# Optimization experiments

Hardware: AMD Instinct MI355X
Metric: run time of the kernel (lower is better)

Reference implementation:

```python
import jax, jax.numpy as jnp
import numpy as np

N_NODES = 50000
N_EDGES = 1600000
F_NODE = 128
F_EDGE = 64
L = 128
EPS = 1e-5


def _bn(h, gamma, beta):
    # BatchNorm1d in training mode: biased batch stats over dim 0
    mu = jnp.mean(h, axis=0, keepdims=True)
    var = jnp.mean((h - mu) ** 2, axis=0, keepdims=True)
    return (h - mu) * jax.lax.rsqrt(var + EPS) * gamma + beta


def setup_inputs() -> dict:
    key = jax.random.key(0)
    ks = jax.random.split(key, 12)
    e1 = F_NODE + F_EDGE          # 192
    e2 = F_NODE + L               # 256
    inp = {
        "x": jax.random.normal(ks[0], (N_NODES, F_NODE), jnp.float32),
        "edge_index": jax.random.randint(ks[1], (2, N_EDGES), 0, N_NODES, jnp.int32),
        "edge_attr": jax.random.normal(ks[2], (N_EDGES, F_EDGE), jnp.float32),
        "u": jax.random.normal(ks[3], (1, 4), jnp.float32),
        "batch": jnp.zeros((N_NODES,), jnp.int32),
        # node_mlp_1: Linear(192 -> 128) + BN + ReLU
        "W1": jax.random.normal(ks[4], (e1, L), jnp.float32) / np.sqrt(e1),
        "b1": jnp.zeros((L,), jnp.float32),
        "g1": jnp.ones((L,), jnp.float32),
        "be1": jnp.zeros((L,), jnp.float32),
        # node_mlp_2: Linear(256 -> 256) + BN + ReLU
        "W2": jax.random.normal(ks[5], (e2, e2), jnp.float32) / np.sqrt(e2),
        "b2": jnp.zeros((e2,), jnp.float32),
        "g2": jnp.ones((e2,), jnp.float32),
        "be2": jnp.zeros((e2,), jnp.float32),
        # linear: 256 -> 128
        "Wl": jax.random.normal(ks[6], (e2, F_NODE), jnp.float32) / np.sqrt(e2),
        "bl": jnp.zeros((F_NODE,), jnp.float32),
    }
    return inp


def reference(x, edge_index, edge_attr, u, batch, W1, b1, g1, be1, W2, b2, g2, be2, Wl, bl):
    n = x.shape[0]
    row, col = edge_index[0], edge_index[1]
    # gather source node feats, concat with edge feats -> [E, F_NODE+F_EDGE]
    h = jnp.concatenate([x[row], edge_attr], axis=1)
    h = jax.nn.relu(_bn(h @ W1 + b1, g1, be1))        # [E, L]
    # scatter-mean over destination nodes
    s = jax.ops.segment_sum(h, col, num_segments=n)   # [N, L]
    cnt = jax.ops.segment_sum(jnp.ones((h.shape[0], 1), h.dtype), col, num_segments=n)
    agg = jnp.where(cnt > 0, s / jnp.maximum(cnt, 1.0), 0.0)
    h2 = jnp.concatenate([x, agg], axis=1)            # [N, F_NODE+L]
    h2 = jax.nn.relu(_bn(h2 @ W2 + b2, g2, be2))
    return jax.nn.relu(h2 @ Wl + bl)                  # [N, F_NODE]
```

## Files before the change

kernel.cpp:

```cpp
#include <hip/hip_runtime.h>
#include <stdint.h>

#define EPSV 1e-5f

typedef short short8 __attribute__((ext_vector_type(8)));
typedef float floatx4 __attribute__((ext_vector_type(4)));

static __device__ __forceinline__ ushort f2b(float f) {
    union { float f; uint32_t u; } v; v.f = f;
    return (ushort)((v.u + 0x7FFFu + ((v.u >> 16) & 1u)) >> 16);
}
static __device__ __forceinline__ uint pack2(float a, float b) {
    return (uint)f2b(a) | ((uint)f2b(b) << 16);
}
static __device__ __forceinline__ float b2f(ushort b) {
    union { uint32_t u; float f; } v; v.u = ((uint32_t)b) << 16;
    return v.f;
}

__global__ void k_prep_w(const float* __restrict__ W, ushort* __restrict__ Wt,
                         int K, int Nc) {
    int i = blockIdx.x * blockDim.x + threadIdx.x;
    if (i >= K * Nc) return;
    int n = i % Nc, k = i / Nc;
    Wt[(size_t)n * K + k] = f2b(W[i]);
}

__global__ void k_prep_x(const float* __restrict__ x, ushort* __restrict__ xb, int n4) {
    int stride = gridDim.x * blockDim.x;
    for (int i = blockIdx.x * blockDim.x + threadIdx.x; i < n4; i += stride) {
        float4 v = ((const float4*)x)[i];
        uint2 o; o.x = pack2(v.x, v.y); o.y = pack2(v.z, v.w);
        ((uint2*)xb)[i] = o;
    }
}

__global__ void k_hist(const int* __restrict__ col, int* __restrict__ deg, int E) {
    int stride = gridDim.x * blockDim.x;
    for (int i = blockIdx.x * blockDim.x + threadIdx.x; i < E; i += stride)
        atomicAdd(&deg[col[i]], 1);
}

__global__ void k_bsum(const int* __restrict__ deg, int* __restrict__ bsum, int Nn) {
    __shared__ int red[256];
    int t = threadIdx.x;
    int i = blockIdx.x * 256 + t;
    red[t] = (i < Nn) ? deg[i] : 0;
    __syncthreads();
    for (int s = 128; s > 0; s >>= 1) {
        if (t < s) red[t] += red[t + s];
        __syncthreads();
    }
    if (t == 0) bsum[blockIdx.x] = red[0];
}

__global__ void k_bscan(const int* __restrict__ bsum, int* __restrict__ bbase, int NB) {
    __shared__ int s[256];
    int t = threadIdx.x;
    int v = (t < NB) ? bsum[t] : 0;
    s[t] = v;
    __syncthreads();
    for (int off = 1; off < 256; off <<= 1) {
        int u = (t >= off) ? s[t - off] : 0;
        __syncthreads();
        s[t] += u;
        __syncthreads();
    }
    if (t < NB) bbase[t] = s[t] - v;
}

__global__ void k_base(const int* __restrict__ deg, const int* __restrict__ bbase,
                       int* __restrict__ base, int Nn) {
    __shared__ int s[256];
    int t = threadIdx.x;
    int i = blockIdx.x * 256 + t;
    int v = (i < Nn) ? deg[i] : 0;
    s[t] = v;
    __syncthreads();
    for (int off = 1; off < 256; off <<= 1) {
        int u = (t >= off) ? s[t - off] : 0;
        __syncthreads();
        s[t] += u;
        __syncthreads();
    }
    if (i < Nn) base[i] = bbase[blockIdx.x] + s[t] - v;
}

__global__ void k_scatter(const int* __restrict__ eidx, const int* __restrict__ base,
                          int* __restrict__ fill, int* __restrict__ perm,
                          int* __restrict__ srcs, int* __restrict__ dsts, int E) {
    int stride = gridDim.x * blockDim.x;
    for (int e = blockIdx.x * blockDim.x + threadIdx.x; e < E; e += stride) {
        int d = eidx[E + e];
        int pos = base[d] + atomicAdd(&fill[d], 1);
        perm[pos] = e;
        if (srcs) { srcs[pos] = eidx[e]; dsts[pos] = d; }
    }
}

__global__ void k_fin(const float* __restrict__ stats, const float* __restrict__ g,
                      const float* __restrict__ be, float* __restrict__ ss,
                      int C, float invM) {
    int c = blockIdx.x * blockDim.x + threadIdx.x;
    if (c >= C) return;
    float mean = stats[c] * invM;
    float var  = stats[C + c] * invM - mean * mean;
    float scale = g[c] * rsqrtf(var + EPSV);
    ss[c] = scale;
    ss[C + c] = be[c] - mean * scale;
}

__global__ void k_fin1(const float* __restrict__ statsB, const float* __restrict__ g,
                       const float* __restrict__ be, float* __restrict__ ss, float invM) {
    int c = threadIdx.x;
    float sm = 0.f, sq = 0.f;
    for (int b = 0; b < 128; ++b) {
        sm += statsB[b * 256 + c];
        sq += statsB[b * 256 + 128 + c];
    }
    float mean = sm * invM;
    float var  = sq * invM - mean * mean;
    float scale = g[c] * rsqrtf(var + EPSV);
    ss[c] = scale;
    ss[128 + c] = be[c] - mean * scale;
}

template <bool BF>
__global__ __launch_bounds__(256) void k_xa(
    const ushort* __restrict__ xb, const ushort* __restrict__ W1t,
    void* __restrict__ out, int Nn)
{
    __shared__ ushort sA[128][72];
    __shared__ ushort sB[128][72];
    const int tid = threadIdx.x;
    const int lane = tid & 63, wave = tid >> 6;
    const int q = lane >> 4, lm = lane & 15;
    const int wr = wave * 32;
    const int rs = tid >> 1;
    const int kh = (tid & 1) * 32;
    const int m0 = blockIdx.x * 128;
    const int row = m0 + rs;
    const bool valid = row < Nn;

    floatx4 acc[2][8];
#pragma unroll
    for (int a = 0; a < 2; ++a)
#pragma unroll
        for (int b = 0; b < 8; ++b) acc[a][b] = (floatx4){0.f, 0.f, 0.f, 0.f};

#pragma unroll
    for (int kc = 0; kc < 2; ++kc) {
        uint4* dstA = (uint4*)&sA[rs][kh];
        const uint4* srcA = (const uint4*)(xb + (size_t)row * 128 + kc * 64 + kh);
#pragma unroll
        for (int j = 0; j < 4; ++j) {
            uint4 o = {0u, 0u, 0u, 0u};
            if (valid) o = srcA[j];
            dstA[j] = o;
        }
        const uint4* srcB = (const uint4*)(W1t + (size_t)rs * 192 + kc * 64 + kh);
        uint4* dstB = (uint4*)&sB[rs][kh];
#pragma unroll
        for (int j = 0; j < 4; ++j) dstB[j] = srcB[j];
        __syncthreads();
#pragma unroll
        for (int ks = 0; ks < 2; ++ks) {
            short8 a0 = *(const short8*)&sA[wr + lm][ks * 32 + q * 8];
            short8 a1 = *(const short8*)&sA[wr + 16 + lm][ks * 32 + q * 8];
#pragma unroll
            for (int ct = 0; ct < 8; ++ct) {
                short8 b = *(const short8*)&sB[ct * 16 + lm][ks * 32 + q * 8];
                acc[0][ct] = __builtin_amdgcn_mfma_f32_16x16x32_bf16(a0, b, acc[0][ct], 0, 0, 0);
                acc[1][ct] = __builtin_amdgcn_mfma_f32_16x16x32_bf16(a1, b, acc[1][ct], 0, 0, 0);
            }
        }
        __syncthreads();
    }
#pragma unroll
    for (int rt = 0; rt < 2; ++rt)
#pragma unroll
        for (int r = 0; r < 4; ++r) {
            int grow = m0 + wr + rt * 16 + q * 4 + r;
            if (grow < Nn) {
                if (BF) {
                    ushort* drow = (ushort*)out + (size_t)grow * 128;
#pragma unroll
                    for (int ct = 0; ct < 8; ++ct)
                        drow[ct * 16 + lm] = f2b(acc[rt][ct][r]);
                } else {
                    float* drow = (float*)out + (size_t)grow * 128;
#pragma unroll
                    for (int ct = 0; ct < 8; ++ct)
                        drow[ct * 16 + lm] = acc[rt][ct][r];
                }
            }
        }
}

__global__ __launch_bounds__(256) void k_edgeA(
    const float* __restrict__ ea, const int* __restrict__ perm,
    const int* __restrict__ srcs, const ushort* __restrict__ W1t,
    const ushort* __restrict__ xab, float* __restrict__ statsB,
    ushort* __restrict__ hs, int E, int NT)
{
    __shared__ union SM {
        struct { ushort A[128][72]; ushort B[128][72]; } t;
        ushort X[128][132];
    } sm;
    __shared__ int sPE[128];
    __shared__ int sSrc[128];
    __shared__ float sRed[256];

    const int tid = threadIdx.x;
    const int lane = tid & 63, wave = tid >> 6;
    const int q = lane >> 4, lm = lane & 15;
    const int wr = wave * 32;
    const int rs = tid >> 1;
    const int half = tid & 1;
    const int kh = half * 32;

    float s1[8], s2[8];
#pragma unroll
    for (int ct = 0; ct < 8; ++ct) { s1[ct] = 0.f; s2[ct] = 0.f; }

    for (int tile = blockIdx.x; tile < NT; tile += gridDim.x) {
        const int e0 = tile * 128;
        __syncthreads();
        if (tid < 128) {
            int e = e0 + tid;
            sPE[tid]  = (e < E) ? perm[e] : -1;
            sSrc[tid] = (e < E) ? srcs[e] : -1;
        }
        __syncthreads();
        {
            int pe = sPE[rs];
            const float4* srcA = (const float4*)(ea + (size_t)pe * 64 + kh);
            uint4* dstA = (uint4*)&sm.t.A[rs][kh];
#pragma unroll
            for (int j = 0; j < 4; ++j) {
                uint4 o = {0u, 0u, 0u, 0u};
                if (pe >= 0) {
                    float4 v0 = srcA[2 * j], v1 = srcA[2 * j + 1];
                    o.x = pack2(v0.x, v0.y); o.y = pack2(v0.z, v0.w);
                    o.z = pack2(v1.x, v1.y); o.w = pack2(v1.z, v1.w);
                }
                dstA[j] = o;
            }
            const uint4* srcB = (const uint4*)(W1t + (size_t)rs * 192 + 128 + kh);
            uint4* dstB = (uint4*)&sm.t.B[rs][kh];
#pragma unroll
            for (int j = 0; j < 4; ++j) dstB[j] = srcB[j];
        }
        __syncthreads();

        floatx4 acc[2][8];
#pragma unroll
        for (int a = 0; a < 2; ++a)
#pragma unroll
            for (int b = 0; b < 8; ++b) acc[a][b] = (floatx4){0.f, 0.f, 0.f, 0.f};
#pragma unroll
        for (int ks = 0; ks < 2; ++ks) {
            short8 a0 = *(const short8*)&sm.t.A[wr + lm][ks * 32 + q * 8];
            short8 a1 = *(const short8*)&sm.t.A[wr + 16 + lm][ks * 32 + q * 8];
#pragma unroll
            for (int ct = 0; ct < 8; ++ct) {
                short8 b = *(const short8*)&sm.t.B[ct * 16 + lm][ks * 32 + q * 8];
                acc[0][ct] = __builtin_amdgcn_mfma_f32_16x16x32_bf16(a0, b, acc[0][ct], 0, 0, 0);
                acc[1][ct] = __builtin_amdgcn_mfma_f32_16x16x32_bf16(a1, b, acc[1][ct], 0, 0, 0);
            }
        }
        __syncthreads();
        {
            int s = sSrc[rs];
            const uint4* gsrc = (const uint4*)(xab + (size_t)(s < 0 ? 0 : s) * 128 + half * 64);
            uint2* ldst = (uint2*)((char*)&sm.X[rs][0] + half * 128);
#pragma unroll
            for (int j = 0; j < 8; ++j) {
                uint4 v = {0u, 0u, 0u, 0u};
                if (s >= 0) v = gsrc[j];
                ldst[2 * j]     = (uint2){v.x, v.y};
                ldst[2 * j + 1] = (uint2){v.z, v.w};
            }
        }
        __syncthreads();
#pragma unroll
        for (int rt = 0; rt < 2; ++rt)
#pragma unroll
            for (int r = 0; r < 4; ++r) {
                int trow = wr + rt * 16 + q * 4 + r;
                if (sPE[trow] >= 0) {
                    ushort* drow = hs + (size_t)(e0 + trow) * 128;
#pragma unroll
                    for (int ct = 0; ct < 8; ++ct) {
                        float v = acc[rt][ct][r] + b2f(sm.X[trow][ct * 16 + lm]);
                        s1[ct] += v; s2[ct] += v * v;
                        drow[ct * 16 + lm] = f2b(v);
                    }
                }
            }
    }

    __syncthreads();
    sRed[tid] = 0.f;
    __syncthreads();
#pragma unroll
    for (int ct = 0; ct < 8; ++ct) {
        float sm2 = s1[ct], sq2 = s2[ct];
        sm2 += __shfl_xor(sm2, 16, 64); sm2 += __shfl_xor(sm2, 32, 64);
        sq2 += __shfl_xor(sq2, 16, 64); sq2 += __shfl_xor(sq2, 32, 64);
        if (q == 0) {
            atomicAdd(&sRed[ct * 16 + lm], sm2);
            atomicAdd(&sRed[128 + ct * 16 + lm], sq2);
        }
    }
    __syncthreads();
    atomicAdd(&statsB[(size_t)(blockIdx.x & 127) * 256 + tid], sRed[tid]);
}

__global__ __launch_bounds__(256) void k_edgeB(
    const ushort* __restrict__ hs, const int* __restrict__ dsts,
    const float* __restrict__ ss, float* __restrict__ sacc, int E, int NT)
{
    __shared__ int sDst[128];
    const int tid = threadIdx.x;
    const int c = tid & 127;
    const int chunk = tid >> 7;
    const float sc = ss[c], sh = ss[128 + c];

    for (int tile = blockIdx.x; tile < NT; tile += gridDim.x) {
        const int e0 = tile * 128;
        __syncthreads();
        if (tid < 128) {
            int e = e0 + tid;
            sDst[tid] = (e < E) ? dsts[e] : -1;
        }
        __syncthreads();
        const int rbeg = chunk * 64;
        int cur = sDst[rbeg];
        float run = 0.f;
#pragma unroll 4
        for (int i = 0; i < 64; ++i) {
            int d = sDst[rbeg + i];
            float v = 0.f;
            if (d >= 0) {
                float hv = b2f(hs[(size_t)(e0 + rbeg + i) * 128 + c]);
                v = fmaxf(fmaf(hv, sc, sh), 0.f);
            }
            if (d != cur) {
                if (cur >= 0) atomicAdd(&sacc[(size_t)cur * 128 + c], run);
                run = 0.f; cur = d;
            }
            run += v;
        }
        if (cur >= 0) atomicAdd(&sacc[(size_t)cur * 128 + c], run);
    }
}

__global__ __launch_bounds__(256) void k_edge1(
    const float* __restrict__ ea, const int* __restrict__ eidx,
    const ushort* __restrict__ W1t, const float* __restrict__ xa,
    float* __restrict__ statsB, int E, int NT)
{
    __shared__ ushort sA[128][72];
    __shared__ ushort sB[128][72];
    __shared__ int sSrc[128];
    __shared__ float sRed[256];

    const int tid = threadIdx.x;
    const int lane = tid & 63, wave = tid >> 6;
    const int q = lane >> 4, lm = lane & 15;
    const int wr = wave * 32;
    const int rs = tid >> 1;
    const int kh = (tid & 1) * 32;

    {
        const uint4* srcB = (const uint4*)(W1t + (size_t)rs * 192 + 128 + kh);
        uint4* dstB = (uint4*)&sB[rs][kh];
#pragma unroll
        for (int j = 0; j < 4; ++j) dstB[j] = srcB[j];
    }

    float s1[8], s2[8];
#pragma unroll
    for (int ct = 0; ct < 8; ++ct) { s1[ct] = 0.f; s2[ct] = 0.f; }

    for (int tile = blockIdx.x; tile < NT; tile += gridDim.x) {
        const int e0 = tile * 128;
        __syncthreads();
        if (tid < 128) {
            int e = e0 + tid;
            sSrc[tid] = (e < E) ? eidx[e] : -1;
        }
        {
            const bool valid = (e0 + rs) < E;
            const float4* srcA = (const float4*)(ea + (size_t)(e0 + rs) * 64 + kh);
            uint4* dstA = (uint4*)&sA[rs][kh];
#pragma unroll
            for (int j = 0; j < 4; ++j) {
                uint4 o = {0u, 0u, 0u, 0u};
                if (valid) {
                    float4 v0 = srcA[2 * j], v1 = srcA[2 * j + 1];
                    o.x = pack2(v0.x, v0.y); o.y = pack2(v0.z, v0.w);
                    o.z = pack2(v1.x, v1.y); o.w = pack2(v1.z, v1.w);
                }
                dstA[j] = o;
            }
        }
        __syncthreads();

        floatx4 acc[2][8];
#pragma unroll
        for (int a = 0; a < 2; ++a)
#pragma unroll
            for (int b = 0; b < 8; ++b) acc[a][b] = (floatx4){0.f, 0.f, 0.f, 0.f};
#pragma unroll
        for (int ks = 0; ks < 2; ++ks) {
            short8 a0 = *(const short8*)&sA[wr + lm][ks * 32 + q * 8];
            short8 a1 = *(const short8*)&sA[wr + 16 + lm][ks * 32 + q * 8];
#pragma unroll
            for (int ct = 0; ct < 8; ++ct) {
                short8 b = *(const short8*)&sB[ct * 16 + lm][ks * 32 + q * 8];
                acc[0][ct] = __builtin_amdgcn_mfma_f32_16x16x32_bf16(a0, b, acc[0][ct], 0, 0, 0);
                acc[1][ct] = __builtin_amdgcn_mfma_f32_16x16x32_bf16(a1, b, acc[1][ct], 0, 0, 0);
            }
        }
#pragma unroll
        for (int rt = 0; rt < 2; ++rt)
#pragma unroll
            for (int r = 0; r < 4; ++r) {
                int trow = wr + rt * 16 + q * 4 + r;
                int srcn = sSrc[trow];
                if (srcn >= 0) {
                    const float* xr = xa + (size_t)srcn * 128 + lm;
#pragma unroll
                    for (int ct = 0; ct < 8; ++ct) {
                        float v = acc[rt][ct][r] + xr[ct * 16];
                        s1[ct] += v; s2[ct] += v * v;
                    }
                }
            }
    }

    __syncthreads();
    sRed[tid] = 0.f;
    __syncthreads();
#pragma unroll
    for (int ct = 0; ct < 8; ++ct) {
        float sm = s1[ct], sq = s2[ct];
        sm += __shfl_xor(sm, 16, 64); sm += __shfl_xor(sm, 32, 64);
        sq += __shfl_xor(sq, 16, 64); sq += __shfl_xor(sq, 32, 64);
        if (q == 0) {
            atomicAdd(&sRed[ct * 16 + lm], sm);
            atomicAdd(&sRed[128 + ct * 16 + lm], sq);
        }
    }
    __syncthreads();
    atomicAdd(&statsB[(size_t)(blockIdx.x & 127) * 256 + tid], sRed[tid]);
}

__global__ __launch_bounds__(256) void k_edge2(
    const float* __restrict__ ea, const int* __restrict__ eidx,
    const int* __restrict__ perm, const ushort* __restrict__ W1t,
    const float* __restrict__ xa, const float* __restrict__ ss,
    float* __restrict__ sacc, int E, int NT)
{
    __shared__ union SM {
        struct { ushort A[128][72]; ushort B[128][72]; } t;
        float buf[64][132];
    } sm;
    __shared__ int sSrc[128];
    __shared__ int sDst[128];

    const int tid = threadIdx.x;
    const int lane = tid & 63, wave = tid >> 6;
    const int q = lane >> 4, lm = lane & 15;
    const int wr = wave * 32;
    const int rs = tid >> 1;
    const int kh = (tid & 1) * 32;

    float sc[8], sh[8];
#pragma unroll
    for (int ct = 0; ct < 8; ++ct) {
        sc[ct] = ss[ct * 16 + lm];
        sh[ct] = ss[128 + ct * 16 + lm];
    }

    for (int tile = blockIdx.x; tile < NT; tile += gridDim.x) {
        const int e0 = tile * 128;
        __syncthreads();
        if (tid < 128) {
            int e = e0 + tid;
            int pe = (e < E) ? perm[e] : -1;
            sSrc[tid] = (pe >= 0) ? eidx[pe] : -1;
            sDst[tid] = (pe >= 0) ? eidx[E + pe] : -1;
        }
        {
            int e = e0 + rs;
            int pe = (e < E) ? perm[e] : -1;
            const float4* srcA = (const float4*)(ea + (size_t)pe * 64 + kh);
            uint4* dstA = (uint4*)&sm.t.A[rs][kh];
#pragma unroll
            for (int j = 0; j < 4; ++j) {
                uint4 o = {0u, 0u, 0u, 0u};
                if (pe >= 0) {
                    float4 v0 = srcA[2 * j], v1 = srcA[2 * j + 1];
                    o.x = pack2(v0.x, v0.y); o.y = pack2(v0.z, v0.w);
                    o.z = pack2(v1.x, v1.y); o.w = pack2(v1.z, v1.w);
                }
                dstA[j] = o;
            }
            const uint4* srcB = (const uint4*)(W1t + (size_t)rs * 192 + 128 + kh);
            uint4* dstB = (uint4*)&sm.t.B[rs][kh];
#pragma unroll
            for (int j = 0; j < 4; ++j) dstB[j] = srcB[j];
        }
        __syncthreads();

        floatx4 acc[2][8];
#pragma unroll
        for (int a = 0; a < 2; ++a)
#pragma unroll
            for (int b = 0; b < 8; ++b) acc[a][b] = (floatx4){0.f, 0.f, 0.f, 0.f};
#pragma unroll
        for (int ks = 0; ks < 2; ++ks) {
            short8 a0 = *(const short8*)&sm.t.A[wr + lm][ks * 32 + q * 8];
            short8 a1 = *(const short8*)&sm.t.A[wr + 16 + lm][ks * 32 + q * 8];
#pragma unroll
            for (int ct = 0; ct < 8; ++ct) {
                short8 b = *(const short8*)&sm.t.B[ct * 16 + lm][ks * 32 + q * 8];
                acc[0][ct] = __builtin_amdgcn_mfma_f32_16x16x32_bf16(a0, b, acc[0][ct], 0, 0, 0);
                acc[1][ct] = __builtin_amdgcn_mfma_f32_16x16x32_bf16(a1, b, acc[1][ct], 0, 0, 0);
            }
        }
#pragma unroll
        for (int rt = 0; rt < 2; ++rt)
#pragma unroll
            for (int r = 0; r < 4; ++r) {
                int trow = wr + rt * 16 + q * 4 + r;
                int srcn = sSrc[trow];
                if (srcn >= 0) {
                    const float* xr = xa + (size_t)srcn * 128 + lm;
#pragma unroll
                    for (int ct = 0; ct < 8; ++ct)
                        acc[rt][ct][r] += xr[ct * 16];
                }
            }

#pragma unroll
        for (int half = 0; half < 2; ++half) {
            __syncthreads();
            if ((wave >> 1) == half) {
                int rb = (wave & 1) * 32;
#pragma unroll
                for (int rt = 0; rt < 2; ++rt)
#pragma unroll
                    for (int r = 0; r < 4; ++r) {
                        int rowl = rb + rt * 16 + q * 4 + r;
#pragma unroll
                        for (int ct = 0; ct < 8; ++ct) {
                            float v = fmaxf(fmaf(acc[rt][ct][r], sc[ct], sh[ct]), 0.f);
                            sm.buf[rowl][ct * 16 + lm] = v;
                        }
                    }
            }
            __syncthreads();
            int c = tid & 127, chunk = tid >> 7;
            int rbeg = half * 64 + chunk * 32;
            int cur = sDst[rbeg];
            float run = 0.f;
#pragma unroll 4
            for (int i = 0; i < 32; ++i) {
                int d = sDst[rbeg + i];
                float v = sm.buf[chunk * 32 + i][c];
                if (d != cur) {
                    if (cur >= 0) atomicAdd(&sacc[(size_t)cur * 128 + c], run);
                    run = 0.f; cur = d;
                }
                run += v;
            }
            if (cur >= 0) atomicAdd(&sacc[(size_t)cur * 128 + c], run);
        }
    }
}

__global__ __launch_bounds__(256) void k_gemm2(
    const ushort* __restrict__ xb, const float* __restrict__ sacc,
    const int* __restrict__ deg, const ushort* __restrict__ W2t,
    float* __restrict__ stats2, ushort* __restrict__ h2, int Nn)
{
    __shared__ ushort sA[128][72];
    __shared__ ushort sB[128][72];
    __shared__ float sRed[256];

    const int tid = threadIdx.x;
    const int m0 = blockIdx.x * 128;
    const int n0 = blockIdx.y * 128;
    const int lane = tid & 63, wave = tid >> 6;
    const int q = lane >> 4, lm = lane & 15;
    const int wr = wave * 32;
    const int rs = tid >> 1;
    const int kh = (tid & 1) * 32;
    const int row = m0 + rs;
    const bool valid = row < Nn;
    float inv = 0.f;
    if (valid) {
        int d = deg[row];
        inv = (d > 0) ? 1.f / (float)d : 0.f;
    }

    floatx4 acc[2][8];
#pragma unroll
    for (int a = 0; a < 2; ++a)
#pragma unroll
        for (int b = 0; b < 8; ++b) acc[a][b] = (floatx4){0.f, 0.f, 0.f, 0.f};

#pragma unroll
    for (int kc = 0; kc < 4; ++kc) {
        uint4* dstA = (uint4*)&sA[rs][kh];
        if (kc < 2) {
            const uint4* src = (const uint4*)(xb + (size_t)row * 128 + kc * 64 + kh);
#pragma unroll
            for (int j = 0; j < 4; ++j) {
                uint4 o = {0u, 0u, 0u, 0u};
                if (valid) o = src[j];
                dstA[j] = o;
            }
        } else {
            const float4* src = (const float4*)(sacc + (size_t)row * 128 + (kc - 2) * 64 + kh);
#pragma unroll
            for (int j = 0; j < 4; ++j) {
                uint4 o = {0u, 0u, 0u, 0u};
                if (valid) {
                    float4 v0 = src[2 * j], v1 = src[2 * j + 1];
                    o.x = pack2(v0.x * inv, v0.y * inv); o.y = pack2(v0.z * inv, v0.w * inv);
                    o.z = pack2(v1.x * inv, v1.y * inv); o.w = pack2(v1.z * inv, v1.w * inv);
                }
                dstA[j] = o;
            }
        }
        {
            const uint4* src = (const uint4*)(W2t + (size_t)(n0 + rs) * 256 + kc * 64 + kh);
            uint4* dstB = (uint4*)&sB[rs][kh];
#pragma unroll
            for (int j = 0; j < 4; ++j) dstB[j] = src[j];
        }
        __syncthreads();
#pragma unroll
        for (int ks = 0; ks < 2; ++ks) {
            short8 a0 = *(const short8*)&sA[wr + lm][ks * 32 + q * 8];
            short8 a1 = *(const short8*)&sA[wr + 16 + lm][ks * 32 + q * 8];
#pragma unroll
            for (int ct = 0; ct < 8; ++ct) {
                short8 b = *(const short8*)&sB[ct * 16 + lm][ks * 32 + q * 8];
                acc[0][ct] = __builtin_amdgcn_mfma_f32_16x16x32_bf16(a0, b, acc[0][ct], 0, 0, 0);
                acc[1][ct] = __builtin_amdgcn_mfma_f32_16x16x32_bf16(a1, b, acc[1][ct], 0, 0, 0);
            }
        }
        __syncthreads();
    }

    sRed[tid] = 0.f;
    __syncthreads();
#pragma unroll
    for (int ct = 0; ct < 8; ++ct) {
        float sm = 0.f, sq = 0.f;
#pragma unroll
        for (int rt = 0; rt < 2; ++rt)
#pragma unroll
            for (int r = 0; r < 4; ++r) {
                float v = acc[rt][ct][r];
                sm += v; sq += v * v;
            }
        sm += __shfl_xor(sm, 16, 64); sm += __shfl_xor(sm, 32, 64);
        sq += __shfl_xor(sq, 16, 64); sq += __shfl_xor(sq, 32, 64);
        if (q == 0) {
            atomicAdd(&sRed[ct * 16 + lm], sm);
            atomicAdd(&sRed[128 + ct * 16 + lm], sq);
        }
    }
#pragma unroll
    for (int rt = 0; rt < 2; ++rt)
#pragma unroll
        for (int r = 0; r < 4; ++r) {
            int grow = m0 + wr + rt * 16 + q * 4 + r;
            if (grow < Nn) {
                ushort* drow = h2 + (size_t)grow * 256 + n0;
#pragma unroll
                for (int ct = 0; ct < 8; ++ct)
                    drow[ct * 16 + lm] = f2b(acc[rt][ct][r]);
            }
        }
    __syncthreads();
    atomicAdd(&stats2[(tid < 128 ? 0 : 256) + n0 + (tid & 127)], sRed[tid]);
}

__global__ __launch_bounds__(256) void k_gemm3(
    const ushort* __restrict__ h2, const float* __restrict__ ss2,
    const ushort* __restrict__ Wlt, const float* __restrict__ bl,
    float* __restrict__ out, int Nn)
{
    __shared__ ushort sA[128][72];
    __shared__ ushort sB[128][72];
    const int tid = threadIdx.x;
    const int m0 = blockIdx.x * 128;
    const int lane = tid & 63, wave = tid >> 6;
    const int q = lane >> 4, lm = lane & 15;
    const int wr = wave * 32;
    const int rs = tid >> 1;
    const int kh = (tid & 1) * 32;
    const int row = m0 + rs;
    const bool valid = row < Nn;

    floatx4 acc[2][8];
#pragma unroll
    for (int a = 0; a < 2; ++a)
#pragma unroll
        for (int b = 0; b < 8; ++b) acc[a][b] = (floatx4){0.f, 0.f, 0.f, 0.f};

#pragma unroll
    for (int kc = 0; kc < 4; ++kc) {
        const int kb = kc * 64 + kh;
        uint4* dstA = (uint4*)&sA[rs][kh];
#pragma unroll
        for (int j = 0; j < 4; ++j) {
            uint4 o = {0u, 0u, 0u, 0u};
            if (valid) {
                uint4 vv = ((const uint4*)(h2 + (size_t)row * 256 + kb))[j];
                uint wds[4] = {vv.x, vv.y, vv.z, vv.w};
                uint res[4];
#pragma unroll
                for (int p = 0; p < 4; ++p) {
                    int k0 = kb + j * 8 + p * 2;
                    float f0 = fmaxf(fmaf(b2f((ushort)(wds[p] & 0xFFFFu)), ss2[k0], ss2[256 + k0]), 0.f);
                    float f1 = fmaxf(fmaf(b2f((ushort)(wds[p] >> 16)), ss2[k0 + 1], ss2[256 + k0 + 1]), 0.f);
                    res[p] = pack2(f0, f1);
                }
                o.x = res[0]; o.y = res[1]; o.z = res[2]; o.w = res[3];
            }
            dstA[j] = o;
        }
        {
            const uint4* src = (const uint4*)(Wlt + (size_t)rs * 256 + kc * 64 + kh);
            uint4* dstB = (uint4*)&sB[rs][kh];
#pragma unroll
            for (int j = 0; j < 4; ++j) dstB[j] = src[j];
        }
        __syncthreads();
#pragma unroll
        for (int ks = 0; ks < 2; ++ks) {
            short8 a0 = *(const short8*)&sA[wr + lm][ks * 32 + q * 8];
            short8 a1 = *(const short8*)&sA[wr + 16 + lm][ks * 32 + q * 8];
#pragma unroll
            for (int ct = 0; ct < 8; ++ct) {
                short8 b = *(const short8*)&sB[ct * 16 + lm][ks * 32 + q * 8];
                acc[0][ct] = __builtin_amdgcn_mfma_f32_16x16x32_bf16(a0, b, acc[0][ct], 0, 0, 0);
                acc[1][ct] = __builtin_amdgcn_mfma_f32_16x16x32_bf16(a1, b, acc[1][ct], 0, 0, 0);
            }
        }
        __syncthreads();
    }

    float bias[8];
#pragma unroll
    for (int ct = 0; ct < 8; ++ct) bias[ct] = bl[ct * 16 + lm];
#pragma unroll
    for (int rt = 0; rt < 2; ++rt)
#pragma unroll
        for (int r = 0; r < 4; ++r) {
            int grow = m0 + wr + rt * 16 + q * 4 + r;
            if (grow < Nn) {
                float* drow = out + (size_t)grow * 128;
#pragma unroll
                for (int ct = 0; ct < 8; ++ct)
                    drow[ct * 16 + lm] = fmaxf(acc[rt][ct][r] + bias[ct], 0.f);
            }
        }
}

extern "C" void kernel_launch(void* const* d_in, const int* in_sizes, int n_in,
                              void* d_out, int out_size, void* d_ws, size_t ws_size,
                              hipStream_t stream) {
    const float* x   = (const float*)d_in[0];
    const int* eidx  = (const int*)d_in[1];
    const float* ea  = (const float*)d_in[2];
    const float* W1  = (const float*)d_in[5];
    const float* g1  = (const float*)d_in[7];
    const float* be1 = (const float*)d_in[8];
    const float* W2  = (const float*)d_in[9];
    const float* g2  = (const float*)d_in[11];
    const float* be2 = (const float*)d_in[12];
    const float* Wl  = (const float*)d_in[13];
    const float* bl  = (const float*)d_in[14];

    const int Nn = in_sizes[0] / 128;
    const int E  = in_sizes[1] / 2;
    const int NB = (Nn + 255) / 256;
    const int NT = (E + 127) / 128;

    char* w = (char*)d_ws;
    float* s_acc   = (float*)w;  w += (size_t)Nn * 128 * 4;
    int*   deg     = (int*)w;    w += (size_t)Nn * 4;
    int*   fill    = (int*)w;    w += (size_t)Nn * 4;
    float* stats1B = (float*)w;  w += (size_t)128 * 256 * 4;
    float* stats2  = (float*)w;  w += 512 * 4;
    size_t zbytes = (size_t)(w - (char*)d_ws);
    float* ss1    = (float*)w;  w += 256 * 4;
    float* ss2    = (float*)w;  w += 512 * 4;
    ushort* W1t   = (ushort*)w; w += 128 * 192 * 2;
    ushort* W2t   = (ushort*)w; w += 256 * 256 * 2;
    ushort* Wlt   = (ushort*)w; w += 128 * 256 * 2;
    ushort* xb    = (ushort*)w; w += (size_t)Nn * 128 * 2;
    ushort* h2    = (ushort*)w; w += (size_t)Nn * 256 * 2;
    int*   base   = (int*)w;    w += (size_t)Nn * 4;
    int*   bsum   = (int*)w;    w += (size_t)NB * 4;
    int*   bbase  = (int*)w;    w += (size_t)NB * 4;
    int*   perm   = (int*)w;    w += (size_t)E * 4;
    int*   srcs_s = (int*)w;    w += (size_t)E * 4;
    int*   dsts_s = (int*)w;    w += (size_t)E * 4;
    ushort* xab   = (ushort*)w; w += (size_t)Nn * 128 * 2;
    float* xa     = (float*)w;  w += (size_t)Nn * 128 * 4;
    size_t need_fb = (size_t)(w - (char*)d_ws);
    ushort* h_s   = (ushort*)w; w += (size_t)E * 128 * 2;
    size_t need_main = (size_t)(w - (char*)d_ws);
    (void)n_in; (void)out_size;

    const bool main_path = (ws_size >= need_main);

    hipMemsetAsync(d_ws, 0, zbytes, stream);

    const int GS = 2048;

    k_prep_w<<<(192 * 128 + 255) / 256, 256, 0, stream>>>(W1, W1t, 192, 128);
    k_prep_w<<<(256 * 256 + 255) / 256, 256, 0, stream>>>(W2, W2t, 256, 256);
    k_prep_w<<<(256 * 128 + 255) / 256, 256, 0, stream>>>(Wl, Wlt, 256, 128);
    k_prep_x<<<GS, 256, 0, stream>>>(x, xb, Nn * 128 / 4);

    k_hist<<<GS, 256, 0, stream>>>(eidx + E, deg, E);
    k_bsum<<<NB, 256, 0, stream>>>(deg, bsum, Nn);
    k_bscan<<<1, 256, 0, stream>>>(bsum, bbase, NB);
    k_base<<<NB, 256, 0, stream>>>(deg, bbase, base, Nn);
    k_scatter<<<GS, 256, 0, stream>>>(eidx, base, fill, perm,
                                      main_path ? srcs_s : nullptr,
                                      main_path ? dsts_s : nullptr, E);

    if (main_path) {
        k_xa<true><<<(Nn + 127) / 128, 256, 0, stream>>>(xb, W1t, (void*)xab, Nn);
        k_edgeA<<<GS, 256, 0, stream>>>(ea, perm, srcs_s, W1t, xab, stats1B, h_s, E, NT);
        k_fin1<<<1, 128, 0, stream>>>(stats1B, g1, be1, ss1, 1.0f / (float)E);
        k_edgeB<<<GS, 256, 0, stream>>>(h_s, dsts_s, ss1, s_acc, E, NT);
    } else {
        (void)need_fb;
        k_xa<false><<<(Nn + 127) / 128, 256, 0, stream>>>(xb, W1t, (void*)xa, Nn);
        k_edge1<<<GS, 256, 0, stream>>>(ea, eidx, W1t, xa, stats1B, E, NT);
        k_fin1<<<1, 128, 0, stream>>>(stats1B, g1, be1, ss1, 1.0f / (float)E);
        k_edge2<<<GS, 256, 0, stream>>>(ea, eidx, perm, W1t, xa, ss1, s_acc, E, NT);
    }

    dim3 grid2((Nn + 127) / 128, 2);
    k_gemm2<<<grid2, 256, 0, stream>>>(xb, s_acc, deg, W2t, stats2, h2, Nn);
    k_fin<<<1, 256, 0, stream>>>(stats2, g2, be2, ss2, 256, 1.0f / (float)Nn);
    k_gemm3<<<(Nn + 127) / 128, 256, 0, stream>>>(h2, ss2, Wlt, bl, (float*)d_out, Nn);
}
```

Baseline: 1.328 ms.

## Permute weight columns so each lane owns 8 contiguous outputs, vectorize stores

Weight rows are permuted during transposition so that each MFMA lane's eight column tiles map to eight contiguous output features. All epilogue stores can then be single 16-byte vector writes, and gathered x rows are read directly per lane in edgeA, which drops the LDS staging pass and two barriers. W1 is also loaded into LDS once per block instead of once per tile, and edgeB reads two columns per thread. Stats, bias and scale indexing are changed throughout to match the new layout, so any site that misses the permutation would produce wrong results.

```diff
diff --git a/kernel.cpp b/kernel.cpp
--- a/kernel.cpp
+++ b/kernel.cpp
@@ -18,12 +18,14 @@
     return v.f;
 }
 
-__global__ void k_prep_w(const float* __restrict__ W, ushort* __restrict__ Wt,
-                         int K, int Nc) {
+__global__ void k_prep_wp(const float* __restrict__ W, ushort* __restrict__ Wt,
+                          int K, int Nc) {
     int i = blockIdx.x * blockDim.x + threadIdx.x;
     if (i >= K * Nc) return;
     int n = i % Nc, k = i / Nc;
-    Wt[(size_t)n * K + k] = f2b(W[i]);
+    int m = n & 127;
+    int r = (n & ~127) + (m & 7) * 16 + (m >> 3);
+    Wt[(size_t)r * K + k] = f2b(W[i]);
 }
 
 __global__ void k_prep_x(const float* __restrict__ x, ushort* __restrict__ xb, int n4) {
@@ -183,15 +185,18 @@
             int grow = m0 + wr + rt * 16 + q * 4 + r;
             if (grow < Nn) {
                 if (BF) {
-                    ushort* drow = (ushort*)out + (size_t)grow * 128;
-#pragma unroll
-                    for (int ct = 0; ct < 8; ++ct)
-                        drow[ct * 16 + lm] = f2b(acc[rt][ct][r]);
+                    uint4 o;
+                    o.x = pack2(acc[rt][0][r], acc[rt][1][r]);
+                    o.y = pack2(acc[rt][2][r], acc[rt][3][r]);
+                    o.z = pack2(acc[rt][4][r], acc[rt][5][r]);
+                    o.w = pack2(acc[rt][6][r], acc[rt][7][r]);
+                    ((uint4*)((ushort*)out + (size_t)grow * 128))[lm] = o;
                 } else {
-                    float* drow = (float*)out + (size_t)grow * 128;
-#pragma unroll
-                    for (int ct = 0; ct < 8; ++ct)
-                        drow[ct * 16 + lm] = acc[rt][ct][r];
+                    float* drow = (float*)out + (size_t)grow * 128 + lm * 8;
+                    float4 f0 = {acc[rt][0][r], acc[rt][1][r], acc[rt][2][r], acc[rt][3][r]};
+                    float4 f1 = {acc[rt][4][r], acc[rt][5][r], acc[rt][6][r], acc[rt][7][r]};
+                    ((float4*)drow)[0] = f0;
+                    ((float4*)drow)[1] = f1;
                 }
             }
         }
@@ -203,11 +208,8 @@
     const ushort* __restrict__ xab, float* __restrict__ statsB,
     ushort* __restrict__ hs, int E, int NT)
 {
-    __shared__ union SM {
-        struct { ushort A[128][72]; ushort B[128][72]; } t;
-        ushort X[128][132];
-    } sm;
-    __shared__ int sPE[128];
+    __shared__ ushort sA[128][72];
+    __shared__ ushort sB[128][72];
     __shared__ int sSrc[128];
     __shared__ float sRed[256];
 
@@ -216,8 +218,14 @@
     const int q = lane >> 4, lm = lane & 15;
     const int wr = wave * 32;
     const int rs = tid >> 1;
-    const int half = tid & 1;
-    const int kh = half * 32;
+    const int kh = (tid & 1) * 32;
+
+    {
+        const uint4* srcB = (const uint4*)(W1t + (size_t)rs * 192 + 128 + kh);
+        uint4* dstB = (uint4*)&sB[rs][kh];
+#pragma unroll
+        for (int j = 0; j < 4; ++j) dstB[j] = srcB[j];
+    }
 
     float s1[8], s2[8];
 #pragma unroll
@@ -228,14 +236,13 @@
         __syncthreads();
         if (tid < 128) {
             int e = e0 + tid;
-            sPE[tid]  = (e < E) ? perm[e] : -1;
             sSrc[tid] = (e < E) ? srcs[e] : -1;
         }
-        __syncthreads();
         {
-            int pe = sPE[rs];
+            int e = e0 + rs;
+            int pe = (e < E) ? perm[e] : -1;
             const float4* srcA = (const float4*)(ea + (size_t)pe * 64 + kh);
-            uint4* dstA = (uint4*)&sm.t.A[rs][kh];
+            uint4* dstA = (uint4*)&sA[rs][kh];
 #pragma unroll
             for (int j = 0; j < 4; ++j) {
                 uint4 o = {0u, 0u, 0u, 0u};
@@ -246,10 +253,6 @@
                 }
                 dstA[j] = o;
             }
-            const uint4* srcB = (const uint4*)(W1t + (size_t)rs * 192 + 128 + kh);
-            uint4* dstB = (uint4*)&sm.t.B[rs][kh];
-#pragma unroll
-            for (int j = 0; j < 4; ++j) dstB[j] = srcB[j];
         }
         __syncthreads();
 
@@ -260,42 +263,36 @@
             for (int b = 0; b < 8; ++b) acc[a][b] = (floatx4){0.f, 0.f, 0.f, 0.f};
 #pragma unroll
         for (int ks = 0; ks < 2; ++ks) {
-            short8 a0 = *(const short8*)&sm.t.A[wr + lm][ks * 32 + q * 8];
-            short8 a1 = *(const short8*)&sm.t.A[wr + 16 + lm][ks * 32 + q * 8];
+            short8 a0 = *(const short8*)&sA[wr + lm][ks * 32 + q * 8];
+            short8 a1 = *(const short8*)&sA[wr + 16 + lm][ks * 32 + q * 8];
 #pragma unroll
             for (int ct = 0; ct < 8; ++ct) {
-                short8 b = *(const short8*)&sm.t.B[ct * 16 + lm][ks * 32 + q * 8];
+                short8 b = *(const short8*)&sB[ct * 16 + lm][ks * 32 + q * 8];
                 acc[0][ct] = __builtin_amdgcn_mfma_f32_16x16x32_bf16(a0, b, acc[0][ct], 0, 0, 0);
                 acc[1][ct] = __builtin_amdgcn_mfma_f32_16x16x32_bf16(a1, b, acc[1][ct], 0, 0, 0);
             }
         }
-        __syncthreads();
-        {
-            int s = sSrc[rs];
-            const uint4* gsrc = (const uint4*)(xab + (size_t)(s < 0 ? 0 : s) * 128 + half * 64);
-            uint2* ldst = (uint2*)((char*)&sm.X[rs][0] + half * 128);
-#pragma unroll
-            for (int j = 0; j < 8; ++j) {
-                uint4 v = {0u, 0u, 0u, 0u};
-                if (s >= 0) v = gsrc[j];
-                ldst[2 * j]     = (uint2){v.x, v.y};
-                ldst[2 * j + 1] = (uint2){v.z, v.w};
-            }
-        }
-        __syncthreads();
 #pragma unroll
         for (int rt = 0; rt < 2; ++rt)
 #pragma unroll
             for (int r = 0; r < 4; ++r) {
                 int trow = wr + rt * 16 + q * 4 + r;
-                if (sPE[trow] >= 0) {
-                    ushort* drow = hs + (size_t)(e0 + trow) * 128;
+                int srcn = sSrc[trow];
+                if (srcn >= 0) {
+                    uint4 g = ((const uint4*)(xab + (size_t)srcn * 128))[lm];
+                    uint gw[4] = {g.x, g.y, g.z, g.w};
+                    float hv[8];
 #pragma unroll
                     for (int ct = 0; ct < 8; ++ct) {
-                        float v = acc[rt][ct][r] + b2f(sm.X[trow][ct * 16 + lm]);
+                        ushort gb = (ushort)(gw[ct >> 1] >> ((ct & 1) * 16));
+                        float v = acc[rt][ct][r] + b2f(gb);
                         s1[ct] += v; s2[ct] += v * v;
-                        drow[ct * 16 + lm] = f2b(v);
+                        hv[ct] = v;
                     }
+                    uint4 o;
+                    o.x = pack2(hv[0], hv[1]); o.y = pack2(hv[2], hv[3]);
+                    o.z = pack2(hv[4], hv[5]); o.w = pack2(hv[6], hv[7]);
+                    ((uint4*)(hs + (size_t)(e0 + trow) * 128))[lm] = o;
                 }
             }
     }
@@ -309,8 +306,8 @@
         sm2 += __shfl_xor(sm2, 16, 64); sm2 += __shfl_xor(sm2, 32, 64);
         sq2 += __shfl_xor(sq2, 16, 64); sq2 += __shfl_xor(sq2, 32, 64);
         if (q == 0) {
-            atomicAdd(&sRed[ct * 16 + lm], sm2);
-            atomicAdd(&sRed[128 + ct * 16 + lm], sq2);
+            atomicAdd(&sRed[lm * 8 + ct], sm2);
+            atomicAdd(&sRed[128 + lm * 8 + ct], sq2);
         }
     }
     __syncthreads();
@@ -323,9 +320,10 @@
 {
     __shared__ int sDst[128];
     const int tid = threadIdx.x;
-    const int c = tid & 127;
-    const int chunk = tid >> 7;
-    const float sc = ss[c], sh = ss[128 + c];
+    const int c0 = (tid & 63) * 2;
+    const int chunk = tid >> 6;
+    const float sc0 = ss[c0],     sh0 = ss[128 + c0];
+    const float sc1 = ss[c0 + 1], sh1 = ss[128 + c0 + 1];
 
     for (int tile = blockIdx.x; tile < NT; tile += gridDim.x) {
         const int e0 = tile * 128;
@@ -335,24 +333,31 @@
             sDst[tid] = (e < E) ? dsts[e] : -1;
         }
         __syncthreads();
-        const int rbeg = chunk * 64;
+        const int rbeg = chunk * 32;
         int cur = sDst[rbeg];
-        float run = 0.f;
+        float r0 = 0.f, r1 = 0.f;
 #pragma unroll 4
-        for (int i = 0; i < 64; ++i) {
+        for (int i = 0; i < 32; ++i) {
             int d = sDst[rbeg + i];
-            float v = 0.f;
+            float v0 = 0.f, v1 = 0.f;
             if (d >= 0) {
-                float hv = b2f(hs[(size_t)(e0 + rbeg + i) * 128 + c]);
-                v = fmaxf(fmaf(hv, sc, sh), 0.f);
+                uint hv = *(const uint*)(hs + (size_t)(e0 + rbeg + i) * 128 + c0);
+                v0 = fmaxf(fmaf(b2f((ushort)(hv & 0xFFFFu)), sc0, sh0), 0.f);
+                v1 = fmaxf(fmaf(b2f((ushort)(hv >> 16)), sc1, sh1), 0.f);
             }
             if (d != cur) {
-                if (cur >= 0) atomicAdd(&sacc[(size_t)cur * 128 + c], run);
-                run = 0.f; cur = d;
-            }
-            run += v;
-        }
-        if (cur >= 0) atomicAdd(&sacc[(size_t)cur * 128 + c], run);
+                if (cur >= 0) {
+                    atomicAdd(&sacc[(size_t)cur * 128 + c0], r0);
+                    atomicAdd(&sacc[(size_t)cur * 128 + c0 + 1], r1);
+                }
+                r0 = 0.f; r1 = 0.f; cur = d;
+            }
+            r0 += v0; r1 += v1;
+        }
+        if (cur >= 0) {
+            atomicAdd(&sacc[(size_t)cur * 128 + c0], r0);
+            atomicAdd(&sacc[(size_t)cur * 128 + c0 + 1], r1);
+        }
     }
 }
 
@@ -431,10 +436,10 @@
                 int trow = wr + rt * 16 + q * 4 + r;
                 int srcn = sSrc[trow];
                 if (srcn >= 0) {
-                    const float* xr = xa + (size_t)srcn * 128 + lm;
+                    const float* xr = xa + (size_t)srcn * 128 + lm * 8;
 #pragma unroll
                     for (int ct = 0; ct < 8; ++ct) {
-                        float v = acc[rt][ct][r] + xr[ct * 16];
+                        float v = acc[rt][ct][r] + xr[ct];
                         s1[ct] += v; s2[ct] += v * v;
                     }
                 }
@@ -450,8 +455,8 @@
         sm += __shfl_xor(sm, 16, 64); sm += __shfl_xor(sm, 32, 64);
         sq += __shfl_xor(sq, 16, 64); sq += __shfl_xor(sq, 32, 64);
         if (q == 0) {
-            atomicAdd(&sRed[ct * 16 + lm], sm);
-            atomicAdd(&sRed[128 + ct * 16 + lm], sq);
+            atomicAdd(&sRed[lm * 8 + ct], sm);
+            atomicAdd(&sRed[128 + lm * 8 + ct], sq);
         }
     }
     __syncthreads();
@@ -481,8 +486,8 @@
     float sc[8], sh[8];
 #pragma unroll
     for (int ct = 0; ct < 8; ++ct) {
-        sc[ct] = ss[ct * 16 + lm];
-        sh[ct] = ss[128 + ct * 16 + lm];
+        sc[ct] = ss[lm * 8 + ct];
+        sh[ct] = ss[128 + lm * 8 + ct];
     }
 
     for (int tile = blockIdx.x; tile < NT; tile += gridDim.x) {
@@ -539,10 +544,10 @@
                 int trow = wr + rt * 16 + q * 4 + r;
                 int srcn = sSrc[trow];
                 if (srcn >= 0) {
-                    const float* xr = xa + (size_t)srcn * 128 + lm;
+                    const float* xr = xa + (size_t)srcn * 128 + lm * 8;
 #pragma unroll
                     for (int ct = 0; ct < 8; ++ct)
-                        acc[rt][ct][r] += xr[ct * 16];
+                        acc[rt][ct][r] += xr[ct];
                 }
             }
 
@@ -559,7 +564,7 @@
 #pragma unroll
                         for (int ct = 0; ct < 8; ++ct) {
                             float v = fmaxf(fmaf(acc[rt][ct][r], sc[ct], sh[ct]), 0.f);
-                            sm.buf[rowl][ct * 16 + lm] = v;
+                            sm.buf[rowl][lm * 8 + ct] = v;
                         }
                     }
             }
@@ -674,8 +679,8 @@
         sm += __shfl_xor(sm, 16, 64); sm += __shfl_xor(sm, 32, 64);
         sq += __shfl_xor(sq, 16, 64); sq += __shfl_xor(sq, 32, 64);
         if (q == 0) {
-            atomicAdd(&sRed[ct * 16 + lm], sm);
-            atomicAdd(&sRed[128 + ct * 16 + lm], sq);
+            atomicAdd(&sRed[lm * 8 + ct], sm);
+            atomicAdd(&sRed[128 + lm * 8 + ct], sq);
         }
     }
 #pragma unroll
@@ -684,10 +689,12 @@
         for (int r = 0; r < 4; ++r) {
             int grow = m0 + wr + rt * 16 + q * 4 + r;
             if (grow < Nn) {
-                ushort* drow = h2 + (size_t)grow * 256 + n0;
-#pragma unroll
-                for (int ct = 0; ct < 8; ++ct)
-                    drow[ct * 16 + lm] = f2b(acc[rt][ct][r]);
+                uint4 o;
+                o.x = pack2(acc[rt][0][r], acc[rt][1][r]);
+                o.y = pack2(acc[rt][2][r], acc[rt][3][r]);
+                o.z = pack2(acc[rt][4][r], acc[rt][5][r]);
+                o.w = pack2(acc[rt][6][r], acc[rt][7][r]);
+                ((uint4*)(h2 + (size_t)grow * 256 + n0))[lm] = o;
             }
         }
     __syncthreads();
@@ -762,17 +769,24 @@
 
     float bias[8];
 #pragma unroll
-    for (int ct = 0; ct < 8; ++ct) bias[ct] = bl[ct * 16 + lm];
+    for (int ct = 0; ct < 8; ++ct) bias[ct] = bl[lm * 8 + ct];
 #pragma unroll
     for (int rt = 0; rt < 2; ++rt)
 #pragma unroll
         for (int r = 0; r < 4; ++r) {
             int grow = m0 + wr + rt * 16 + q * 4 + r;
             if (grow < Nn) {
-                float* drow = out + (size_t)grow * 128;
-#pragma unroll
-                for (int ct = 0; ct < 8; ++ct)
-                    drow[ct * 16 + lm] = fmaxf(acc[rt][ct][r] + bias[ct], 0.f);
+                float* drow = out + (size_t)grow * 128 + lm * 8;
+                float4 f0 = {fmaxf(acc[rt][0][r] + bias[0], 0.f),
+                             fmaxf(acc[rt][1][r] + bias[1], 0.f),
+                             fmaxf(acc[rt][2][r] + bias[2], 0.f),
+                             fmaxf(acc[rt][3][r] + bias[3], 0.f)};
+                float4 f1 = {fmaxf(acc[rt][4][r] + bias[4], 0.f),
+                             fmaxf(acc[rt][5][r] + bias[5], 0.f),
+                             fmaxf(acc[rt][6][r] + bias[6], 0.f),
+                             fmaxf(acc[rt][7][r] + bias[7], 0.f)};
+                ((float4*)drow)[0] = f0;
+                ((float4*)drow)[1] = f1;
             }
         }
 }
@@ -830,9 +844,9 @@
 
     const int GS = 2048;
 
-    k_prep_w<<<(192 * 128 + 255) / 256, 256, 0, stream>>>(W1, W1t, 192, 128);
-    k_prep_w<<<(256 * 256 + 255) / 256, 256, 0, stream>>>(W2, W2t, 256, 256);
-    k_prep_w<<<(256 * 128 + 255) / 256, 256, 0, stream>>>(Wl, Wlt, 256, 128);
+    k_prep_wp<<<(192 * 128 + 255) / 256, 256, 0, stream>>>(W1, W1t, 192, 128);
+    k_prep_wp<<<(256 * 256 + 255) / 256, 256, 0, stream>>>(W2, W2t, 256, 256);
+    k_prep_wp<<<(256 * 128 + 255) / 256, 256, 0, stream>>>(Wl, Wlt, 256, 128);
     k_prep_x<<<GS, 256, 0, stream>>>(x, xb, Nn * 128 / 4);
 
     k_hist<<<GS, 256, 0, stream>>>(eidx + E, deg, E);
```

New measurement: 1.182 ms. 1.12x faster.
